# Kernel optimization log

Measured on AMD Instinct MI355X. Metric: run time of the kernel, lower is better.

Reference implementation:

```python
import jax, jax.numpy as jnp
import numpy as np

NUM_EMB = 1024
EMB_DIM = 256
COMMIT = 0.25
EPS = 1e-12  # matches torch F.normalize eps


def _l2norm(x):
    return x / jnp.maximum(jnp.linalg.norm(x, axis=-1, keepdims=True), EPS)


def setup_inputs() -> dict:
    key = jax.random.key(0)
    k1, k2 = jax.random.split(key)
    inputs = jax.random.normal(k1, (64, 256, 32, 32), dtype=jnp.float32)
    weight = jax.random.uniform(k2, (NUM_EMB, EMB_DIM), dtype=jnp.float32,
                                minval=-1.0 / NUM_EMB, maxval=1.0 / NUM_EMB)
    return {"inputs": inputs, "weight": weight}


def reference(inputs, weight):
    B, D, H, W = inputs.shape
    x = jnp.transpose(inputs, (0, 2, 3, 1))           # [B,H,W,D]
    flat = x.reshape(-1, D)                           # [N,D]
    fn = _l2norm(flat)                                # normalized inputs
    wn = _l2norm(weight)                              # normalized codebook [K,D]
    # squared euclidean distances between unit vectors
    dist = (jnp.sum(fn * fn, axis=1, keepdims=True)
            + jnp.sum(wn * wn, axis=1)
            - 2.0 * fn @ wn.T)                        # [N,K]
    idx = jnp.argmin(dist, axis=1)                    # [N]
    quant = wn[idx].reshape(x.shape)                  # codebook gather == onehot @ wn
    inorm = fn.reshape(x.shape)
    e_loss = jnp.mean((jax.lax.stop_gradient(quant) - inorm) ** 2)
    q_loss = jnp.mean((quant - jax.lax.stop_gradient(inorm)) ** 2)
    loss = q_loss + COMMIT * e_loss
    quant_st = inorm + jax.lax.stop_gradient(quant - inorm)  # straight-through
    return loss, jnp.transpose(quant_st, (0, 3, 1, 2)), idx[:, None]
```

## Files before the change

### kernel.cpp

```cpp
#include <hip/hip_runtime.h>
#include <math.h>

#define NUM_EMB 1024
#define EMB_DIM 256
#define N_ROWS  65536
#define HW      1024
#define QUANT_OFF 1
#define IDX_OFF   (1 + 16777216)
#define LDA 264

typedef unsigned int uint;
typedef _Float16 f16x8 __attribute__((ext_vector_type(8)));
typedef float    f32x4 __attribute__((ext_vector_type(4)));

__device__ __forceinline__ uint umin2(uint a, uint b) { return a < b ? a : b; }
__device__ __forceinline__ uint umax2(uint a, uint b) { return a > b ? a : b; }

__device__ __forceinline__ uint umed3(uint a, uint b, uint c) {
  uint d;
  asm("v_med3_u32 %0, %1, %2, %3" : "=v"(d) : "v"(a), "v"(b), "v"(c));
  return d;
}

__device__ __forceinline__ void load_lds16(const _Float16* g, _Float16* l) {
  __builtin_amdgcn_global_load_lds(
      (const __attribute__((address_space(1))) unsigned int*)g,
      (__attribute__((address_space(3))) unsigned int*)l, 16, 0, 0);
}

__global__ __launch_bounds__(256)
void k_norm_w(const float* __restrict__ w, float* __restrict__ wn,
              _Float16* __restrict__ wh2, double* __restrict__ rinv) {
  const int k = blockIdx.x, t = threadIdx.x;
  const float v = w[(size_t)k * EMB_DIM + t];
  double s = (double)v * (double)v;
  for (int o = 32; o; o >>= 1) s += __shfl_down(s, o);
  __shared__ double ps[4];
  if ((t & 63) == 0) ps[t >> 6] = s;
  __syncthreads();
  const double tot = ps[0] + ps[1] + ps[2] + ps[3];
  const float nv = v / fmaxf((float)sqrt(tot), 1e-12f);
  wn[(size_t)k * EMB_DIM + t] = nv;
  const int chunk = k >> 8, cc = k & 255;
  const int ks = t >> 5, q = (t >> 3) & 3, e = t & 7;
  wh2[(size_t)chunk * 65536 + ks * 8192 + q * 2048 + cc * 8 + e] = (_Float16)nv;
  if (t == 0) rinv[k] = 1.0 / fmax(sqrt(tot), 1e-12);
}

__global__ __launch_bounds__(256)
void k_pass1(const float* __restrict__ x, const _Float16* __restrict__ wh2,
             uint* __restrict__ cand) {
  __shared__ __align__(16) _Float16 As[64 * LDA];
  __shared__ __align__(16) _Float16 Bs[2][8192];
  const int t = threadIdx.x;
  const int blk = blockIdx.x;
  const int b = blk >> 4;
  const int hw0 = (blk & 15) * 64;

  {
    const _Float16* slab = wh2 + (size_t)t * 8;
    _Float16* dst = &Bs[0][t * 8];
#pragma unroll
    for (int i = 0; i < 4; ++i)
      load_lds16(slab + i * 2048, dst + i * 2048);
  }

  {
    const int lhw = t & 63;
    const int ph = t >> 6;
    const float* xb = x + (size_t)b * (EMB_DIM * HW) + hw0 + lhw;
#pragma unroll
    for (int jp = 0; jp < 8; ++jp) {
      const int d0 = ph * 64 + jp * 8;
      f16x8 v;
#pragma unroll
      for (int e = 0; e < 8; ++e)
        v[e] = (_Float16)xb[(size_t)(d0 + e) * HW];
      *(f16x8*)&As[lhw * LDA + d0] = v;
    }
  }

  const int lane = t & 63;
  const int q = lane >> 4;
  const int l15 = lane & 15;
  const int w = t >> 6;

  uint t1[16], t2[16];
#pragma unroll
  for (int i = 0; i < 16; ++i) { t1[i] = 0u; t2[i] = 0u; }

  __syncthreads();

  int cur = 0;
  for (int c4 = 0; c4 < 4; ++c4) {
    f32x4 acc[4][4];
#pragma unroll
    for (int rt = 0; rt < 4; ++rt)
#pragma unroll
      for (int ct = 0; ct < 4; ++ct) acc[rt][ct] = (f32x4)0.f;

#pragma unroll 1
    for (int ks = 0; ks < 8; ++ks) {
      const int s = c4 * 8 + ks;
      if (s < 31) {
        const int sn = s + 1;
        const _Float16* slab = wh2 + (size_t)(sn >> 3) * 65536 + (sn & 7) * 8192 + t * 8;
        _Float16* dst = &Bs[cur ^ 1][t * 8];
#pragma unroll
        for (int i = 0; i < 4; ++i)
          load_lds16(slab + i * 2048, dst + i * 2048);
      }

      const f16x8 a0 = *(const f16x8*)&As[(0 * 16 + l15) * LDA + ks * 32 + q * 8];
      const f16x8 a1 = *(const f16x8*)&As[(1 * 16 + l15) * LDA + ks * 32 + q * 8];
      const f16x8 a2 = *(const f16x8*)&As[(2 * 16 + l15) * LDA + ks * 32 + q * 8];
      const f16x8 a3 = *(const f16x8*)&As[(3 * 16 + l15) * LDA + ks * 32 + q * 8];
      const f16x8 b0 = *(const f16x8*)&Bs[cur][q * 2048 + (w * 64 +  0 + l15) * 8];
      const f16x8 b1 = *(const f16x8*)&Bs[cur][q * 2048 + (w * 64 + 16 + l15) * 8];
      const f16x8 b2 = *(const f16x8*)&Bs[cur][q * 2048 + (w * 64 + 32 + l15) * 8];
      const f16x8 b3 = *(const f16x8*)&Bs[cur][q * 2048 + (w * 64 + 48 + l15) * 8];
      acc[0][0] = __builtin_amdgcn_mfma_f32_16x16x32_f16(a0, b0, acc[0][0], 0, 0, 0);
      acc[1][0] = __builtin_amdgcn_mfma_f32_16x16x32_f16(a1, b0, acc[1][0], 0, 0, 0);
      acc[2][0] = __builtin_amdgcn_mfma_f32_16x16x32_f16(a2, b0, acc[2][0], 0, 0, 0);
      acc[3][0] = __builtin_amdgcn_mfma_f32_16x16x32_f16(a3, b0, acc[3][0], 0, 0, 0);
      acc[0][1] = __builtin_amdgcn_mfma_f32_16x16x32_f16(a0, b1, acc[0][1], 0, 0, 0);
      acc[1][1] = __builtin_amdgcn_mfma_f32_16x16x32_f16(a1, b1, acc[1][1], 0, 0, 0);
      acc[2][1] = __builtin_amdgcn_mfma_f32_16x16x32_f16(a2, b1, acc[2][1], 0, 0, 0);
      acc[3][1] = __builtin_amdgcn_mfma_f32_16x16x32_f16(a3, b1, acc[3][1], 0, 0, 0);
      acc[0][2] = __builtin_amdgcn_mfma_f32_16x16x32_f16(a0, b2, acc[0][2], 0, 0, 0);
      acc[1][2] = __builtin_amdgcn_mfma_f32_16x16x32_f16(a1, b2, acc[1][2], 0, 0, 0);
      acc[2][2] = __builtin_amdgcn_mfma_f32_16x16x32_f16(a2, b2, acc[2][2], 0, 0, 0);
      acc[3][2] = __builtin_amdgcn_mfma_f32_16x16x32_f16(a3, b2, acc[3][2], 0, 0, 0);
      acc[0][3] = __builtin_amdgcn_mfma_f32_16x16x32_f16(a0, b3, acc[0][3], 0, 0, 0);
      acc[1][3] = __builtin_amdgcn_mfma_f32_16x16x32_f16(a1, b3, acc[1][3], 0, 0, 0);
      acc[2][3] = __builtin_amdgcn_mfma_f32_16x16x32_f16(a2, b3, acc[2][3], 0, 0, 0);
      acc[3][3] = __builtin_amdgcn_mfma_f32_16x16x32_f16(a3, b3, acc[3][3], 0, 0, 0);

      __syncthreads();
      cur ^= 1;
    }

#pragma unroll
    for (int ct = 0; ct < 4; ++ct) {
      const uint idxv = (uint)(c4 * 256 + w * 64 + ct * 16 + l15);
#pragma unroll
      for (int rt = 0; rt < 4; ++rt)
#pragma unroll
        for (int r = 0; r < 4; ++r) {
          const float v = fmaxf(acc[rt][ct][r], 0.0f);
          const uint key = (__float_as_uint(v) & 0xFFFFFC00u) | idxv;
          const int slot = rt * 4 + r;
          t2[slot] = umed3(key, t1[slot], t2[slot]);
          t1[slot] = umax2(key, t1[slot]);
        }
    }
  }

  __syncthreads();
  uint* keys = (uint*)As;
#pragma unroll
  for (int slot = 0; slot < 16; ++slot) {
    const int rt = slot >> 2, r = slot & 3;
    const int row = rt * 16 + q * 4 + r;
    const int col = w * 32 + l15 * 2;
    keys[row * 128 + col] = t1[slot];
    keys[row * 128 + col + 1] = t2[slot];
  }
  __syncthreads();
  {
    const int row = t >> 2, seg = t & 3;
    uint s1 = 0, s2 = 0;
#pragma unroll
    for (int i = 0; i < 8; ++i) {
      const int ii = (i + t) & 7;
      const uint4 k4 = *(const uint4*)&keys[row * 128 + seg * 32 + ii * 4];
      const uint kk[4] = {k4.x, k4.y, k4.z, k4.w};
#pragma unroll
      for (int e = 0; e < 4; ++e) {
        s2 = umed3(kk[e], s1, s2);
        s1 = umax2(kk[e], s1);
      }
    }
    __syncthreads();
    keys[t * 2] = s1;
    keys[t * 2 + 1] = s2;
  }
  __syncthreads();
  if (t < 64) {
    uint c0 = 0, c1 = 0, c2 = 0, c3 = 0;
#pragma unroll
    for (int i = 0; i < 8; ++i) {
      const uint k = keys[t * 8 + i];
      const uint n0 = umin2(c0, k); c0 = umax2(c0, k);
      const uint n1 = umin2(c1, n0); c1 = umax2(c1, n0);
      const uint n2 = umin2(c2, n1); c2 = umax2(c2, n1);
      c3 = umax2(c3, n2);
    }
    uint4 o; o.x = c0; o.y = c1; o.z = c2; o.w = c3;
    *(uint4*)&cand[(size_t)(blk * 64 + t) * 4] = o;
  }
}

#define XSTR 257
__global__ __launch_bounds__(256)
void k_finish(const float* __restrict__ x, const float* __restrict__ w,
              const float* __restrict__ wn, const double* __restrict__ rinv,
              const uint* __restrict__ cand, float* __restrict__ out) {
  __shared__ float smem[256 * 33];
  __shared__ double lsum[4];
  const int t = threadIdx.x;
  const int blk = blockIdx.x;
  const int b = blk >> 5;
  const int hw0 = (blk & 31) * 32;

  {
    const int r = t & 31, dp = t >> 5;
    const float* xb = x + (size_t)b * (EMB_DIM * HW) + hw0 + r;
#pragma unroll
    for (int j = 0; j < 32; ++j) {
      const int d = dp * 32 + j;
      smem[r * XSTR + d] = xb[(size_t)d * HW];
    }
  }
  __syncthreads();

  const int row = t >> 3;
  const int li = t & 7;
  const int n0 = blk * 32 + row;
  const uint4 ck = *(const uint4*)&cand[(size_t)n0 * 4];
  const uint cv[4] = {ck.x, ck.y, ck.z, ck.w};

  float xf[32];
#pragma unroll
  for (int k = 0; k < 8; ++k)
#pragma unroll
    for (int e = 0; e < 4; ++e)
      xf[k * 4 + e] = smem[row * XSTR + k * 32 + li * 4 + e];
  __syncthreads();

  double sxx = 0.0;
#pragma unroll
  for (int i = 0; i < 32; ++i) sxx = fma((double)xf[i], (double)xf[i], sxx);

  double sj[4];
#pragma unroll
  for (int j = 0; j < 4; ++j) {
    const int c = (int)(cv[j] & 1023u);
    const float* wr = w + (size_t)c * EMB_DIM;
    double s = 0.0;
#pragma unroll
    for (int k = 0; k < 8; ++k) {
      const float4 w4 = *(const float4*)&wr[k * 32 + li * 4];
      const float wv[4] = {w4.x, w4.y, w4.z, w4.w};
#pragma unroll
      for (int e = 0; e < 4; ++e)
        s = fma((double)xf[k * 4 + e], (double)wv[e], s);
    }
    sj[j] = s;
  }

#pragma unroll
  for (int o = 4; o; o >>= 1) {
    sxx += __shfl_down(sxx, o);
#pragma unroll
    for (int j = 0; j < 4; ++j) sj[j] += __shfl_down(sj[j], o);
  }

  double dmin = 0.0;
  int cw = 0;
  if (li == 0) {
    double qbest = -1e300; cw = 1 << 30;
#pragma unroll
    for (int j = 0; j < 4; ++j) {
      const int c = (int)(cv[j] & 1023u);
      const double qj = sj[j] * rinv[c];
      if (qj > qbest || (qj == qbest && c < cw)) { qbest = qj; cw = c; }
    }
    dmin = 2.0 - 2.0 * qbest / fmax(sqrt(sxx), 1e-12);
    out[IDX_OFF + n0] = (float)cw;
  }
  cw = __shfl(cw, (t & 63) & ~7);

  double v = dmin;
  v += __shfl_down(v, 32);
  v += __shfl_down(v, 16);
  v += __shfl_down(v, 8);
  if ((t & 63) == 0) lsum[t >> 6] = v;
  __syncthreads();
  if (t == 0)
    atomicAdd(out, (float)(1.25 * (lsum[0] + lsum[1] + lsum[2] + lsum[3]) / 16777216.0));

  {
    const float* wr = wn + (size_t)cw * EMB_DIM;
#pragma unroll
    for (int k = 0; k < 8; ++k) {
      const int d0 = k * 32 + li * 4;
      const float4 w4 = *(const float4*)&wr[d0];
      smem[(d0 + 0) * 33 + row] = w4.x;
      smem[(d0 + 1) * 33 + row] = w4.y;
      smem[(d0 + 2) * 33 + row] = w4.z;
      smem[(d0 + 3) * 33 + row] = w4.w;
    }
  }
  __syncthreads();
  {
    const int hw4 = (t & 7) * 4, dbase = t >> 3;
    float* qout = out + QUANT_OFF + (size_t)b * (EMB_DIM * HW) + hw0;
#pragma unroll
    for (int jj = 0; jj < 8; ++jj) {
      const int d = jj * 32 + dbase;
      float4 v4;
      v4.x = smem[d * 33 + hw4 + 0];
      v4.y = smem[d * 33 + hw4 + 1];
      v4.z = smem[d * 33 + hw4 + 2];
      v4.w = smem[d * 33 + hw4 + 3];
      *(float4*)&qout[(size_t)d * HW + hw4] = v4;
    }
  }
}

extern "C" void kernel_launch(void* const* d_in, const int* in_sizes, int n_in,
                              void* d_out, int out_size, void* d_ws, size_t ws_size,
                              hipStream_t stream) {
  const float* x = (const float*)d_in[0];
  const float* w = (const float*)d_in[1];
  float* out = (float*)d_out;

  char* ws = (char*)d_ws;
  float*     wn   = (float*)ws;
  _Float16*  wh2  = (_Float16*)(ws + 1048576);
  double*    rinv = (double*)(ws + 1048576 + 524288);
  uint*      cand = (uint*)(ws + 1048576 + 524288 + 8192);

  hipMemsetAsync(d_out, 0, sizeof(float), stream);
  hipLaunchKernelGGL(k_norm_w, dim3(NUM_EMB), dim3(256), 0, stream, w, wn, wh2, rinv);
  hipLaunchKernelGGL(k_pass1, dim3(N_ROWS / 64), dim3(256), 0, stream, x, wh2, cand);
  hipLaunchKernelGGL(k_finish, dim3(N_ROWS / 32), dim3(256), 0, stream, x, w, wn, rinv, cand, out);
}
```

Before: 203.8 us.

## Stream codebook fragments from global into registers and halve pass1 row tile

Pass1 now processes 32 rows per block instead of 64. It keeps the A fragments resident in registers and loads the codebook B fragments straight from global/L2 into double-buffered registers, with no LDS staging and no per-step barriers. LDS usage falls sharply and launch bounds ask for 2 blocks per SM, with twice as many blocks in the grid. The trade-off is that every wave re-fetches the whole codebook from global memory, so L2 traffic goes up and reuse per fetch goes down.

```diff
diff --git a/kernel.cpp b/kernel.cpp
--- a/kernel.cpp
+++ b/kernel.cpp
@@ -20,12 +20,6 @@
   uint d;
   asm("v_med3_u32 %0, %1, %2, %3" : "=v"(d) : "v"(a), "v"(b), "v"(c));
   return d;
-}
-
-__device__ __forceinline__ void load_lds16(const _Float16* g, _Float16* l) {
-  __builtin_amdgcn_global_load_lds(
-      (const __attribute__((address_space(1))) unsigned int*)g,
-      (__attribute__((address_space(3))) unsigned int*)l, 16, 0, 0);
 }
 
 __global__ __launch_bounds__(256)
@@ -47,104 +41,87 @@
   if (t == 0) rinv[k] = 1.0 / fmax(sqrt(tot), 1e-12);
 }
 
-__global__ __launch_bounds__(256)
+__global__ __launch_bounds__(256, 2)
 void k_pass1(const float* __restrict__ x, const _Float16* __restrict__ wh2,
              uint* __restrict__ cand) {
-  __shared__ __align__(16) _Float16 As[64 * LDA];
-  __shared__ __align__(16) _Float16 Bs[2][8192];
+  __shared__ __align__(16) _Float16 As[32 * LDA];
   const int t = threadIdx.x;
   const int blk = blockIdx.x;
-  const int b = blk >> 4;
-  const int hw0 = (blk & 15) * 64;
-
-  {
-    const _Float16* slab = wh2 + (size_t)t * 8;
-    _Float16* dst = &Bs[0][t * 8];
-#pragma unroll
-    for (int i = 0; i < 4; ++i)
-      load_lds16(slab + i * 2048, dst + i * 2048);
-  }
-
-  {
-    const int lhw = t & 63;
-    const int ph = t >> 6;
-    const float* xb = x + (size_t)b * (EMB_DIM * HW) + hw0 + lhw;
-#pragma unroll
-    for (int jp = 0; jp < 8; ++jp) {
-      const int d0 = ph * 64 + jp * 8;
-      f16x8 v;
-#pragma unroll
-      for (int e = 0; e < 8; ++e)
-        v[e] = (_Float16)xb[(size_t)(d0 + e) * HW];
-      *(f16x8*)&As[lhw * LDA + d0] = v;
-    }
-  }
+  const int b = blk >> 5;
+  const int hw0 = (blk & 31) * 32;
 
   const int lane = t & 63;
   const int q = lane >> 4;
   const int l15 = lane & 15;
   const int w = t >> 6;
 
-  uint t1[16], t2[16];
-#pragma unroll
-  for (int i = 0; i < 16; ++i) { t1[i] = 0u; t2[i] = 0u; }
-
-  __syncthreads();
-
-  int cur = 0;
+  const int bvo0 = q * 2048 + (w * 64 +  0 + l15) * 8;
+  const int bvo1 = q * 2048 + (w * 64 + 16 + l15) * 8;
+  const int bvo2 = q * 2048 + (w * 64 + 32 + l15) * 8;
+  const int bvo3 = q * 2048 + (w * 64 + 48 + l15) * 8;
+
+#define LOADB(buf, cc, kk)                                            \
+  { const _Float16* ksb_ = wh2 + (size_t)((cc) * 8 + (kk)) * 8192;    \
+    buf[0] = *(const f16x8*)&ksb_[bvo0];                              \
+    buf[1] = *(const f16x8*)&ksb_[bvo1];                              \
+    buf[2] = *(const f16x8*)&ksb_[bvo2];                              \
+    buf[3] = *(const f16x8*)&ksb_[bvo3]; }
+
+  f16x8 bb[2][4];
+  LOADB(bb[0], 0, 0);
+
+  {
+    const int r = t & 31;
+    const int dp = t >> 5;
+    const float* xb = x + (size_t)b * (EMB_DIM * HW) + hw0 + r;
+#pragma unroll
+    for (int jp = 0; jp < 4; ++jp) {
+      const int d0 = dp * 32 + jp * 8;
+      f16x8 v;
+#pragma unroll
+      for (int e = 0; e < 8; ++e)
+        v[e] = (_Float16)xb[(size_t)(d0 + e) * HW];
+      *(f16x8*)&As[r * LDA + d0] = v;
+    }
+  }
+  __syncthreads();
+
+  f16x8 areg[2][8];
+#pragma unroll
+  for (int rt = 0; rt < 2; ++rt)
+#pragma unroll
+    for (int ks = 0; ks < 8; ++ks)
+      areg[rt][ks] = *(const f16x8*)&As[(rt * 16 + l15) * LDA + ks * 32 + q * 8];
+
+  uint t1[8], t2[8];
+#pragma unroll
+  for (int i = 0; i < 8; ++i) { t1[i] = 0u; t2[i] = 0u; }
+
+#pragma unroll
   for (int c4 = 0; c4 < 4; ++c4) {
-    f32x4 acc[4][4];
-#pragma unroll
-    for (int rt = 0; rt < 4; ++rt)
+    f32x4 acc[2][4];
+#pragma unroll
+    for (int rt = 0; rt < 2; ++rt)
 #pragma unroll
       for (int ct = 0; ct < 4; ++ct) acc[rt][ct] = (f32x4)0.f;
 
-#pragma unroll 1
+#pragma unroll
     for (int ks = 0; ks < 8; ++ks) {
-      const int s = c4 * 8 + ks;
-      if (s < 31) {
-        const int sn = s + 1;
-        const _Float16* slab = wh2 + (size_t)(sn >> 3) * 65536 + (sn & 7) * 8192 + t * 8;
-        _Float16* dst = &Bs[cur ^ 1][t * 8];
-#pragma unroll
-        for (int i = 0; i < 4; ++i)
-          load_lds16(slab + i * 2048, dst + i * 2048);
+      const int cb = ks & 1, nb = cb ^ 1;
+      if (ks < 7) { LOADB(bb[nb], c4, ks + 1); }
+      else if (c4 < 3) { LOADB(bb[nb], c4 + 1, 0); }
+#pragma unroll
+      for (int ct = 0; ct < 4; ++ct) {
+        acc[0][ct] = __builtin_amdgcn_mfma_f32_16x16x32_f16(areg[0][ks], bb[cb][ct], acc[0][ct], 0, 0, 0);
+        acc[1][ct] = __builtin_amdgcn_mfma_f32_16x16x32_f16(areg[1][ks], bb[cb][ct], acc[1][ct], 0, 0, 0);
       }
-
-      const f16x8 a0 = *(const f16x8*)&As[(0 * 16 + l15) * LDA + ks * 32 + q * 8];
-      const f16x8 a1 = *(const f16x8*)&As[(1 * 16 + l15) * LDA + ks * 32 + q * 8];
-      const f16x8 a2 = *(const f16x8*)&As[(2 * 16 + l15) * LDA + ks * 32 + q * 8];
-      const f16x8 a3 = *(const f16x8*)&As[(3 * 16 + l15) * LDA + ks * 32 + q * 8];
-      const f16x8 b0 = *(const f16x8*)&Bs[cur][q * 2048 + (w * 64 +  0 + l15) * 8];
-      const f16x8 b1 = *(const f16x8*)&Bs[cur][q * 2048 + (w * 64 + 16 + l15) * 8];
-      const f16x8 b2 = *(const f16x8*)&Bs[cur][q * 2048 + (w * 64 + 32 + l15) * 8];
-      const f16x8 b3 = *(const f16x8*)&Bs[cur][q * 2048 + (w * 64 + 48 + l15) * 8];
-      acc[0][0] = __builtin_amdgcn_mfma_f32_16x16x32_f16(a0, b0, acc[0][0], 0, 0, 0);
-      acc[1][0] = __builtin_amdgcn_mfma_f32_16x16x32_f16(a1, b0, acc[1][0], 0, 0, 0);
-      acc[2][0] = __builtin_amdgcn_mfma_f32_16x16x32_f16(a2, b0, acc[2][0], 0, 0, 0);
-      acc[3][0] = __builtin_amdgcn_mfma_f32_16x16x32_f16(a3, b0, acc[3][0], 0, 0, 0);
-      acc[0][1] = __builtin_amdgcn_mfma_f32_16x16x32_f16(a0, b1, acc[0][1], 0, 0, 0);
-      acc[1][1] = __builtin_amdgcn_mfma_f32_16x16x32_f16(a1, b1, acc[1][1], 0, 0, 0);
-      acc[2][1] = __builtin_amdgcn_mfma_f32_16x16x32_f16(a2, b1, acc[2][1], 0, 0, 0);
-      acc[3][1] = __builtin_amdgcn_mfma_f32_16x16x32_f16(a3, b1, acc[3][1], 0, 0, 0);
-      acc[0][2] = __builtin_amdgcn_mfma_f32_16x16x32_f16(a0, b2, acc[0][2], 0, 0, 0);
-      acc[1][2] = __builtin_amdgcn_mfma_f32_16x16x32_f16(a1, b2, acc[1][2], 0, 0, 0);
-      acc[2][2] = __builtin_amdgcn_mfma_f32_16x16x32_f16(a2, b2, acc[2][2], 0, 0, 0);
-      acc[3][2] = __builtin_amdgcn_mfma_f32_16x16x32_f16(a3, b2, acc[3][2], 0, 0, 0);
-      acc[0][3] = __builtin_amdgcn_mfma_f32_16x16x32_f16(a0, b3, acc[0][3], 0, 0, 0);
-      acc[1][3] = __builtin_amdgcn_mfma_f32_16x16x32_f16(a1, b3, acc[1][3], 0, 0, 0);
-      acc[2][3] = __builtin_amdgcn_mfma_f32_16x16x32_f16(a2, b3, acc[2][3], 0, 0, 0);
-      acc[3][3] = __builtin_amdgcn_mfma_f32_16x16x32_f16(a3, b3, acc[3][3], 0, 0, 0);
-
-      __syncthreads();
-      cur ^= 1;
     }
 
 #pragma unroll
     for (int ct = 0; ct < 4; ++ct) {
       const uint idxv = (uint)(c4 * 256 + w * 64 + ct * 16 + l15);
 #pragma unroll
-      for (int rt = 0; rt < 4; ++rt)
+      for (int rt = 0; rt < 2; ++rt)
 #pragma unroll
         for (int r = 0; r < 4; ++r) {
           const float v = fmaxf(acc[rt][ct][r], 0.0f);
@@ -155,11 +132,12 @@
         }
     }
   }
+#undef LOADB
 
   __syncthreads();
   uint* keys = (uint*)As;
 #pragma unroll
-  for (int slot = 0; slot < 16; ++slot) {
+  for (int slot = 0; slot < 8; ++slot) {
     const int rt = slot >> 2, r = slot & 3;
     const int row = rt * 16 + q * 4 + r;
     const int col = w * 32 + l15 * 2;
@@ -168,12 +146,12 @@
   }
   __syncthreads();
   {
-    const int row = t >> 2, seg = t & 3;
+    const int row = t >> 3, seg = t & 7;
     uint s1 = 0, s2 = 0;
 #pragma unroll
-    for (int i = 0; i < 8; ++i) {
-      const int ii = (i + t) & 7;
-      const uint4 k4 = *(const uint4*)&keys[row * 128 + seg * 32 + ii * 4];
+    for (int i = 0; i < 4; ++i) {
+      const int ii = (i + t) & 3;
+      const uint4 k4 = *(const uint4*)&keys[row * 128 + seg * 16 + ii * 4];
       const uint kk[4] = {k4.x, k4.y, k4.z, k4.w};
 #pragma unroll
       for (int e = 0; e < 4; ++e) {
@@ -186,18 +164,18 @@
     keys[t * 2 + 1] = s2;
   }
   __syncthreads();
-  if (t < 64) {
+  if (t < 32) {
     uint c0 = 0, c1 = 0, c2 = 0, c3 = 0;
 #pragma unroll
-    for (int i = 0; i < 8; ++i) {
-      const uint k = keys[t * 8 + i];
+    for (int i = 0; i < 16; ++i) {
+      const uint k = keys[t * 16 + i];
       const uint n0 = umin2(c0, k); c0 = umax2(c0, k);
       const uint n1 = umin2(c1, n0); c1 = umax2(c1, n0);
       const uint n2 = umin2(c2, n1); c2 = umax2(c2, n1);
       c3 = umax2(c3, n2);
     }
     uint4 o; o.x = c0; o.y = c1; o.z = c2; o.w = c3;
-    *(uint4*)&cand[(size_t)(blk * 64 + t) * 4] = o;
+    *(uint4*)&cand[(size_t)(blk * 32 + t) * 4] = o;
   }
 }
 
@@ -334,6 +312,6 @@
 
   hipMemsetAsync(d_out, 0, sizeof(float), stream);
   hipLaunchKernelGGL(k_norm_w, dim3(NUM_EMB), dim3(256), 0, stream, w, wn, wh2, rinv);
-  hipLaunchKernelGGL(k_pass1, dim3(N_ROWS / 64), dim3(256), 0, stream, x, wh2, cand);
+  hipLaunchKernelGGL(k_pass1, dim3(N_ROWS / 32), dim3(256), 0, stream, x, wh2, cand);
   hipLaunchKernelGGL(k_finish, dim3(N_ROWS / 32), dim3(256), 0, stream, x, w, wn, rinv, cand, out);
 }
```

New measurement: 195.6 us. 4.0% less time.
